# Kernel optimization log

Measured on AMD Instinct MI355X. Metric: run time of the kernel, lower is better.

The kernel has to match this reference:

```python
import jax, jax.numpy as jnp
import numpy as np

# ultralytics ops.non_max_suppression defaults
CONF_THRES = 0.25
IOU_THRES = 0.45
MAX_DET = 300          # max detections returned per image
MAX_WH = 7680.0        # class-offset constant for class-aware NMS
MAX_NMS = 1024         # fixed candidate cap (ultralytics uses 30000; fixed-size for jit)


def _xywh2xyxy(x):
    # x: [..., 4] (cx, cy, w, h) -> (x1, y1, x2, y2)
    xy, half_wh = x[..., :2], x[..., 2:] * 0.5
    return jnp.concatenate([xy - half_wh, xy + half_wh], axis=-1)


def _pairwise_iou(b):
    # b: [K, 4] xyxy -> [K, K] IoU
    area = (b[:, 2] - b[:, 0]) * (b[:, 3] - b[:, 1])
    lt = jnp.maximum(b[:, None, :2], b[None, :, :2])
    rb = jnp.minimum(b[:, None, 2:], b[None, :, 2:])
    wh = jnp.clip(rb - lt, 0.0)
    inter = wh[..., 0] * wh[..., 1]
    return inter / (area[:, None] + area[None, :] - inter + 1e-7)


def _nms_single(pred):
    # pred: [4+nc, N] raw detector output for one image
    boxes = _xywh2xyxy(pred[:4].T)          # [N, 4]
    scores = pred[4:].T                     # [N, nc]
    conf = scores.max(axis=-1)              # [N]
    cls = scores.argmax(axis=-1).astype(pred.dtype)  # [N]

    valid = conf > CONF_THRES
    masked_conf = jnp.where(valid, conf, -1.0)
    top_conf, idx = jax.lax.top_k(masked_conf, MAX_NMS)   # sorted desc
    b = boxes[idx]                          # [K, 4]
    c = cls[idx]                            # [K]

    # class-aware NMS via coordinate offset per class
    iou = _pairwise_iou(b + c[:, None] * MAX_WH)          # [K, K]

    keep0 = top_conf > CONF_THRES
    ar = jnp.arange(MAX_NMS)

    def body(i, keep):
        # greedy: if box i is kept, suppress all lower-scored boxes with high IoU
        sup = keep[i] & (iou[i] > IOU_THRES) & (ar > i)
        return keep & ~sup

    keep = jax.lax.fori_loop(0, MAX_NMS, body, keep0)

    kept_conf = jnp.where(keep, top_conf, -1.0)
    det_conf, di = jax.lax.top_k(kept_conf, MAX_DET)
    det = jnp.concatenate(
        [b[di], det_conf[:, None], c[di][:, None]], axis=-1)  # [MAX_DET, 6]
    ok = (det_conf > CONF_THRES)[:, None]
    return jnp.where(ok, det, 0.0)


def setup_inputs() -> dict:
    key = jax.random.key(0)
    # [batch, 4+nc, num_anchors]: xywh in [0,1), class scores in [0,1)
    preds = jax.random.uniform(key, (32, 84, 8400), dtype=jnp.float32)
    return {"preds": preds}


def reference(preds):
    dets = jax.vmap(_nms_single)(preds)  # [B, MAX_DET, 6] (xyxy, conf, cls)
    return dets[0]                       # module returns preds[0]
```

## Files before the change

### kernel.cpp

```cpp
#include <hip/hip_runtime.h>
#include <cstdint>
#include <cstddef>


#define NA    8400
#define NCLS  80
#define NTOP  1024
#define NDET  300
#define CONF_T 0.25f
#define IOU_T  0.45f
#define MAXWH  7680.0f

#define NSLICE 25
#define SLICEW 336

#define OFF_KEY   0
#define OFF_CLS   33600
#define OFF_CONF  67200
#define OFF_SCONF 100800
#define OFF_SX1   104896
#define OFF_SY1   108992
#define OFF_SX2   113088
#define OFF_SY2   117184
#define OFF_SCLS  121280
#define OFF_SUP   125376
#define OFF_RANK  256448

typedef unsigned long long u64;
typedef unsigned int u32;

__device__ __forceinline__ int sw(int j) { return j + (j >> 6); }

__device__ __forceinline__ u32 f2mono(float f) {
    u32 u = __float_as_uint(f);
    return u ^ ((u & 0x80000000u) ? 0xFFFFFFFFu : 0x80000000u);
}
__device__ __forceinline__ float mono2f(u32 m) {
    u32 u = (m & 0x80000000u) ? (m ^ 0x80000000u) : ~m;
    return __uint_as_float(u);
}
__device__ __forceinline__ u64 rl64(u64 v, int g) {
    u32 lo = (u32)__builtin_amdgcn_readlane((int)(u32)v, g);
    u32 hi = (u32)__builtin_amdgcn_readlane((int)(u32)(v >> 32), g);
    return ((u64)hi << 32) | lo;
}

__global__ __launch_bounds__(1024) void k_confcls(const float* __restrict__ pred,
                                                  u32* __restrict__ key,
                                                  float* __restrict__ clsf,
                                                  float* __restrict__ conf,
                                                  u32* __restrict__ rank)
{
    __shared__ u64 pk[8][128];
    int tid = threadIdx.x;
    int q = tid >> 7, t = tid & 127;
    int a = blockIdx.x * 128 + t;
    u64 pv = 0ULL;
    if (a < NA) {
        const float* s = pred + (size_t)(4 + q * 10) * NA;
        float best = s[a];
        int bc = q * 10;
#pragma unroll
        for (int c = 1; c < 10; ++c) {
            float v = s[(size_t)c * NA + a];
            if (v > best) { best = v; bc = q * 10 + c; }
        }
        pv = ((u64)f2mono(best) << 32) | (u32)(255 - bc);
    }
    pk[q][t] = pv;
    __syncthreads();
    if (q == 0 && a < NA) {
        u64 mm = pk[0][t];
#pragma unroll
        for (int r = 1; r < 8; ++r) { u64 v = pk[r][t]; if (v > mm) mm = v; }
        float best = mono2f((u32)(mm >> 32));
        int bc = 255 - (int)(mm & 0xFFu);
        float m = (best > CONF_T) ? best : -1.0f;
        key[a]  = ~f2mono(m);
        clsf[a] = (float)bc;
        conf[a] = m;
        rank[a] = 0u;
    }
}

__global__ __launch_bounds__(256) void k_rank_partial(const u32* __restrict__ key,
                                                      u32* __restrict__ rank)
{
    __shared__ __align__(16) u32 kh[SLICEW];
    int tid = threadIdx.x;
    int s   = blockIdx.y;
    int jb  = s * SLICEW;
    for (int k = tid; k < SLICEW; k += 256) kh[k] = key[jb + k];
    __syncthreads();

    int a = blockIdx.x * 256 + tid;
    if (a >= NA) return;

    u64 myk = (((u64)key[a]) << 32) | (u32)a;
    u32 r = 0;
    const uint4* kv4 = (const uint4*)kh;
#pragma unroll 4
    for (int j4 = 0; j4 < SLICEW / 4; ++j4) {
        uint4 kk = kv4[j4];
        u32 j = (u32)jb + (u32)j4 * 4u;
        r += ((((u64)kk.x) << 32) | (j + 0u)) < myk;
        r += ((((u64)kk.y) << 32) | (j + 1u)) < myk;
        r += ((((u64)kk.z) << 32) | (j + 2u)) < myk;
        r += ((((u64)kk.w) << 32) | (j + 3u)) < myk;
    }
    atomicAdd(&rank[a], r);
}

__global__ __launch_bounds__(256) void k_scatter(const float* __restrict__ pred,
                                                 const u32* __restrict__ rank,
                                                 const float* __restrict__ clsf,
                                                 const float* __restrict__ conf,
                                                 float* __restrict__ wsf)
{
    int a = blockIdx.x * 256 + threadIdx.x;
    if (a >= NA) return;
    u32 r = rank[a];
    if (r < NTOP) {
#pragma clang fp contract(off)
        float x = pred[0 * NA + a], y = pred[1 * NA + a];
        float w = pred[2 * NA + a], h = pred[3 * NA + a];
        float hw = w * 0.5f, hh = h * 0.5f;
        wsf[OFF_SCONF / 4 + r] = conf[a];
        wsf[OFF_SX1  / 4 + r] = x - hw;
        wsf[OFF_SY1  / 4 + r] = y - hh;
        wsf[OFF_SX2  / 4 + r] = x + hw;
        wsf[OFF_SY2  / 4 + r] = y + hh;
        wsf[OFF_SCLS / 4 + r] = clsf[a];
    }
}

__global__ __launch_bounds__(256) void k_supmat(const float* __restrict__ wsf,
                                                u64* __restrict__ sup)
{
#pragma clang fp contract(off)
    __shared__ float4 obox[NTOP + 16];
    __shared__ float  oar[NTOP + 16];
    int tid = threadIdx.x;
    for (int k = tid; k < NTOP; k += 256) {
        float cls = wsf[OFF_SCLS / 4 + k];
        float off = cls * MAXWH;
        float x1 = wsf[OFF_SX1 / 4 + k] + off;
        float y1 = wsf[OFF_SY1 / 4 + k] + off;
        float x2 = wsf[OFF_SX2 / 4 + k] + off;
        float y2 = wsf[OFF_SY2 / 4 + k] + off;
        int si = sw(k);
        obox[si] = make_float4(x1, y1, x2, y2);
        oar[si]  = (x2 - x1) * (y2 - y1);
    }
    __syncthreads();

    int gid = blockIdx.x * 256 + tid;
    int i = gid >> 4;
    int l = gid & 15;
    int si = sw(i);
    float4 bb = obox[si];
    float  ba = oar[si];
    u64 bits = 0ULL;
    int j0 = l << 6;
#pragma unroll 4
    for (int jj = 0; jj < 64; ++jj) {
        int j = j0 + jj;
        int sj = sw(j);
        float4 ob = obox[sj];
        float xx1 = fmaxf(bb.x, ob.x);
        float yy1 = fmaxf(bb.y, ob.y);
        float xx2 = fminf(bb.z, ob.z);
        float yy2 = fminf(bb.w, ob.w);
        float w  = fmaxf(xx2 - xx1, 0.0f);
        float hh = fmaxf(yy2 - yy1, 0.0f);
        float inter = w * hh;
        float denom = ba + oar[sj] - inter + 1e-7f;
        bool s = (j > i) && ((inter / denom) > IOU_T);
        bits |= ((u64)s) << jj;
    }
    sup[(size_t)i * 16 + l] = bits;
}

__global__ __launch_bounds__(1024) void k_nms_out(const float* __restrict__ wsf,
                                                  const u64* __restrict__ sup,
                                                  float* __restrict__ out)
{
    __shared__ u64 lsup[NTOP * 16];
    __shared__ u64 tg[16 * 64];
    __shared__ u64 lkeep[64];
    __shared__ u64 kc[16];
    __shared__ u32 pcs[16];
    int tid  = threadIdx.x;
    int lane = tid & 63;
    int wv   = tid >> 6;

    {
        const uint4* gs = (const uint4*)sup;
        uint4* lv = (uint4*)lsup;
        for (int idx = tid; idx < NTOP * 8; idx += 1024) {
            uint4 v = gs[idx];
            lv[idx] = v;
            int row = idx >> 3;
            int c   = (idx & 7) * 2;
            int g   = row >> 6;
            if (c == g)     tg[(g << 6) + (row & 63)] = (((u64)v.y) << 32) | v.x;
            if (c + 1 == g) tg[(g << 6) + (row & 63)] = (((u64)v.w) << 32) | v.z;
        }
    }

    u64 bl = __ballot(wsf[OFF_SCONF / 4 + tid] > CONF_T);
    if (lane == 0) kc[wv] = bl;
    __syncthreads();

    if (wv == 0) {
        int l   = lane & 15;
        int rep = lane >> 4;
        u64 keep = kc[l];
        for (int g = 0; g < 16; ++g) {
            u64 scur = rl64(keep, g) & rl64(keep, 16 + g) &
                       rl64(keep, 32 + g) & rl64(keep, 48 + g);
            u64 rgv = tg[(g << 6) + lane];
#pragma unroll
            for (int ii = 0; ii < 64; ++ii) {
                u64 rg  = rl64(rgv, ii);
                u64 sel = 0ULL - ((scur >> ii) & 1ULL);
                scur &= ~(rg & sel);
            }
#pragma unroll 4
            for (int b = 0; b < 16; ++b) {
                int i_loc = (b << 2) + rep;
                u64 rl = lsup[(((g << 6) + i_loc) << 4) + l];
                u64 m  = 0ULL - ((scur >> i_loc) & 1ULL);
                keep &= ~(rl & m);
            }
        }
        lkeep[lane] = keep;
    }
    __syncthreads();

    if (tid < 16) {
        u64 kk = lkeep[tid] & lkeep[16 + tid] & lkeep[32 + tid] & lkeep[48 + tid];
        kc[tid]  = kk;
        pcs[tid] = (u32)__popcll(kk);
    }
    __syncthreads();

    if (tid < NDET) {
        int acc = 0, chunk = -1, off = 0;
#pragma unroll
        for (int c = 0; c < 16; ++c) {
            int p = (int)pcs[c];
            if (chunk < 0 && tid < acc + p) { chunk = c; off = tid - acc; }
            acc += p;
        }
        float o0 = 0.f, o1 = 0.f, o2 = 0.f, o3 = 0.f, o4 = 0.f, o5 = 0.f;
        if (chunk >= 0) {
            u64 mk = kc[chunk];
            for (int q = 0; q < off; ++q) mk &= mk - 1ULL;
            int p = chunk * 64 + __builtin_ctzll(mk);
            o0 = wsf[OFF_SX1  / 4 + p];
            o1 = wsf[OFF_SY1  / 4 + p];
            o2 = wsf[OFF_SX2  / 4 + p];
            o3 = wsf[OFF_SY2  / 4 + p];
            o4 = wsf[OFF_SCONF / 4 + p];
            o5 = wsf[OFF_SCLS / 4 + p];
        }
        out[tid * 6 + 0] = o0; out[tid * 6 + 1] = o1; out[tid * 6 + 2] = o2;
        out[tid * 6 + 3] = o3; out[tid * 6 + 4] = o4; out[tid * 6 + 5] = o5;
    }
}

extern "C" void kernel_launch(void* const* d_in, const int* in_sizes, int n_in,
                              void* d_out, int out_size, void* d_ws, size_t ws_size,
                              hipStream_t stream)
{
    const float* preds = (const float*)d_in[0];
    char* ws = (char*)d_ws;
    u32* key    = (u32*)(ws + OFF_KEY);
    float* clsf = (float*)(ws + OFF_CLS);
    float* conf = (float*)(ws + OFF_CONF);
    float* wsf  = (float*)ws;
    u64* sup    = (u64*)(ws + OFF_SUP);
    u32* rank   = (u32*)(ws + OFF_RANK);
    float* out  = (float*)d_out;

    hipLaunchKernelGGL(k_confcls,      dim3(66),         dim3(1024), 0, stream, preds, key, clsf, conf, rank);
    hipLaunchKernelGGL(k_rank_partial, dim3(33, NSLICE), dim3(256),  0, stream, key, rank);
    hipLaunchKernelGGL(k_scatter,      dim3(33),         dim3(256),  0, stream, preds, rank, clsf, conf, wsf);
    hipLaunchKernelGGL(k_supmat,       dim3(64),         dim3(256),  0, stream, wsf, sup);
    hipLaunchKernelGGL(k_nms_out,      dim3(1),          dim3(1024), 0, stream, wsf, sup, out);
}
```

Before: 170.1 us.

## Fuse top-K scatter into suppression-matrix kernel and halve confcls block size

The separate scatter kernel is removed. Each k_supmat block now scans all 8400 anchors' ranks and builds the offset boxes for the top 1024 directly in shared memory, and block 0 also writes the sorted candidate arrays used by the final NMS kernel. This saves one kernel launch and the global round trip through the workspace, at the cost of every one of the 64 blocks reading the rank and box arrays redundantly. The conf/class kernel is also reshaped from 66 blocks of 1024 threads to 132 blocks of 512 to spread the work over more CUs.

```diff
diff --git a/kernel.cpp b/kernel.cpp
--- a/kernel.cpp
+++ b/kernel.cpp
@@ -45,16 +45,16 @@
     return ((u64)hi << 32) | lo;
 }
 
-__global__ __launch_bounds__(1024) void k_confcls(const float* __restrict__ pred,
-                                                  u32* __restrict__ key,
-                                                  float* __restrict__ clsf,
-                                                  float* __restrict__ conf,
-                                                  u32* __restrict__ rank)
-{
-    __shared__ u64 pk[8][128];
+__global__ __launch_bounds__(512) void k_confcls(const float* __restrict__ pred,
+                                                 u32* __restrict__ key,
+                                                 float* __restrict__ clsf,
+                                                 float* __restrict__ conf,
+                                                 u32* __restrict__ rank)
+{
+    __shared__ u64 pk[8][64];
     int tid = threadIdx.x;
-    int q = tid >> 7, t = tid & 127;
-    int a = blockIdx.x * 128 + t;
+    int q = tid >> 6, t = tid & 63;
+    int a = blockIdx.x * 64 + t;
     u64 pv = 0ULL;
     if (a < NA) {
         const float* s = pred + (size_t)(4 + q * 10) * NA;
@@ -111,46 +111,41 @@
     atomicAdd(&rank[a], r);
 }
 
-__global__ __launch_bounds__(256) void k_scatter(const float* __restrict__ pred,
-                                                 const u32* __restrict__ rank,
-                                                 const float* __restrict__ clsf,
-                                                 const float* __restrict__ conf,
-                                                 float* __restrict__ wsf)
-{
-    int a = blockIdx.x * 256 + threadIdx.x;
-    if (a >= NA) return;
-    u32 r = rank[a];
-    if (r < NTOP) {
-#pragma clang fp contract(off)
-        float x = pred[0 * NA + a], y = pred[1 * NA + a];
-        float w = pred[2 * NA + a], h = pred[3 * NA + a];
-        float hw = w * 0.5f, hh = h * 0.5f;
-        wsf[OFF_SCONF / 4 + r] = conf[a];
-        wsf[OFF_SX1  / 4 + r] = x - hw;
-        wsf[OFF_SY1  / 4 + r] = y - hh;
-        wsf[OFF_SX2  / 4 + r] = x + hw;
-        wsf[OFF_SY2  / 4 + r] = y + hh;
-        wsf[OFF_SCLS / 4 + r] = clsf[a];
-    }
-}
-
-__global__ __launch_bounds__(256) void k_supmat(const float* __restrict__ wsf,
+__global__ __launch_bounds__(256) void k_supmat(const float* __restrict__ pred,
+                                                const u32* __restrict__ rank,
+                                                const float* __restrict__ clsf,
+                                                const float* __restrict__ conf,
+                                                float* __restrict__ wsf,
                                                 u64* __restrict__ sup)
 {
 #pragma clang fp contract(off)
     __shared__ float4 obox[NTOP + 16];
     __shared__ float  oar[NTOP + 16];
     int tid = threadIdx.x;
-    for (int k = tid; k < NTOP; k += 256) {
-        float cls = wsf[OFF_SCLS / 4 + k];
-        float off = cls * MAXWH;
-        float x1 = wsf[OFF_SX1 / 4 + k] + off;
-        float y1 = wsf[OFF_SY1 / 4 + k] + off;
-        float x2 = wsf[OFF_SX2 / 4 + k] + off;
-        float y2 = wsf[OFF_SY2 / 4 + k] + off;
-        int si = sw(k);
-        obox[si] = make_float4(x1, y1, x2, y2);
-        oar[si]  = (x2 - x1) * (y2 - y1);
+    bool b0 = (blockIdx.x == 0);
+    for (int a = tid; a < NA; a += 256) {
+        u32 r = rank[a];
+        if (r < NTOP) {
+            float x = pred[a], y = pred[NA + a];
+            float w = pred[2 * NA + a], h = pred[3 * NA + a];
+            float cls = clsf[a];
+            float hw = w * 0.5f, hh = h * 0.5f;
+            float x1 = x - hw, y1 = y - hh, x2 = x + hw, y2 = y + hh;
+            float off = cls * MAXWH;
+            float ox1 = x1 + off, oy1 = y1 + off;
+            float ox2 = x2 + off, oy2 = y2 + off;
+            int si = sw((int)r);
+            obox[si] = make_float4(ox1, oy1, ox2, oy2);
+            oar[si]  = (ox2 - ox1) * (oy2 - oy1);
+            if (b0) {
+                wsf[OFF_SCONF / 4 + r] = conf[a];
+                wsf[OFF_SX1  / 4 + r] = x1;
+                wsf[OFF_SY1  / 4 + r] = y1;
+                wsf[OFF_SX2  / 4 + r] = x2;
+                wsf[OFF_SY2  / 4 + r] = y2;
+                wsf[OFF_SCLS / 4 + r] = cls;
+            }
+        }
     }
     __syncthreads();
 
@@ -284,9 +279,8 @@
     u32* rank   = (u32*)(ws + OFF_RANK);
     float* out  = (float*)d_out;
 
-    hipLaunchKernelGGL(k_confcls,      dim3(66),         dim3(1024), 0, stream, preds, key, clsf, conf, rank);
+    hipLaunchKernelGGL(k_confcls,      dim3(132),        dim3(512),  0, stream, preds, key, clsf, conf, rank);
     hipLaunchKernelGGL(k_rank_partial, dim3(33, NSLICE), dim3(256),  0, stream, key, rank);
-    hipLaunchKernelGGL(k_scatter,      dim3(33),         dim3(256),  0, stream, preds, rank, clsf, conf, wsf);
-    hipLaunchKernelGGL(k_supmat,       dim3(64),         dim3(256),  0, stream, wsf, sup);
+    hipLaunchKernelGGL(k_supmat,       dim3(64),         dim3(256),  0, stream, preds, rank, clsf, conf, wsf, sup);
     hipLaunchKernelGGL(k_nms_out,      dim3(1),          dim3(1024), 0, stream, wsf, sup, out);
 }
```

New measurement: 189.6 us. +11.5%, slower.
